# Kernel optimization log

Measured on AMD Instinct MI355X. Metric: run time of the kernel, lower is better.

Reference implementation:

```python
import jax, jax.numpy as jnp
import numpy as np

DIMEN = (341, 341, 341, 341, 341, 343)  # sums to 2048
MARGIN = 0.3
EPS = 1e-12
# index map expanding the 6 per-group attention weights to 2048 feature dims
_EXPAND_IDX = np.repeat(np.arange(len(DIMEN)), DIMEN)  # (2048,)


def setup_inputs() -> dict:
    key = jax.random.key(0)
    k1, k2, k3 = jax.random.split(key, 3)
    inputs = jax.random.normal(k1, (64, 2048), dtype=jnp.float32)
    targets = jax.random.randint(k2, (64,), 0, 16, dtype=jnp.int64)
    attention_attribute = jax.random.uniform(k3, (64, 64, 6), dtype=jnp.float32)
    return {"inputs": inputs, "targets": targets, "attention_attribute": attention_attribute}


def reference(inputs, targets, attention_attribute):
    n = inputs.shape[0]  # 64
    # expand (n,n,6) group weights to (n,n,2048) per-feature weights
    w = attention_attribute[:, :, _EXPAND_IDX]
    # weighted pairwise squared distance: sum_k (w_ijk*(f_jk - f_ik))^2
    diff = inputs[None, :, :] - inputs[:, None, :]  # (n,n,2048)
    sq = jnp.sum((w * diff) ** 2, axis=2)  # (n,n)
    dist = jnp.sqrt(jnp.clip(sq, EPS))  # dist_pos == dist_neg in original
    mask = targets[:, None] == targets[None, :]  # (n,n) bool
    dist_ap = jnp.max(jnp.where(mask, dist, -jnp.inf), axis=1)  # hardest positive
    dist_an = jnp.min(jnp.where(mask, jnp.inf, dist), axis=1)   # hardest negative
    # MarginRankingLoss with y=1: mean(relu(-(dist_an - dist_ap) + margin))
    loss = jnp.mean(jax.nn.relu(dist_ap - dist_an + MARGIN))
    return loss
```

## Files before the change

kernel.cpp:

```cpp
#include <hip/hip_runtime.h>
#include <math.h>


__global__ __launch_bounds__(256) void pair_dist_kernel(
    const float* __restrict__ x,
    const float* __restrict__ attr,
    float* __restrict__ dist)
{
    const int wid  = blockIdx.x * 4 + (threadIdx.x >> 6);
    const int lane = threadIdx.x & 63;
    const int i    = wid >> 6;
    const int j    = wid & 63;

    const float4* __restrict__ xi = (const float4*)(x + i * 2048);
    const float4* __restrict__ xj = (const float4*)(x + j * 2048);
    const float*  __restrict__ a  = attr + wid * 6;

    const float a20 = a[0] * a[0];
    const float a21 = a[1] * a[1];
    const float a22 = a[2] * a[2];
    const float a23 = a[3] * a[3];
    const float a24 = a[4] * a[4];
    const float a25 = a[5] * a[5];

    float acc = 0.f;

#define STEP_B(T, WLO, WHI, B)                                               \
    {                                                                        \
        const int c  = (T) * 64 + lane;                                      \
        const int k0 = c * 4;                                                \
        float4 vi = xi[c];                                                   \
        float4 vj = xj[c];                                                   \
        float dx;                                                            \
        dx = vj.x - vi.x; acc = fmaf(dx * dx, (k0 + 0 < (B)) ? (WLO) : (WHI), acc); \
        dx = vj.y - vi.y; acc = fmaf(dx * dx, (k0 + 1 < (B)) ? (WLO) : (WHI), acc); \
        dx = vj.z - vi.z; acc = fmaf(dx * dx, (k0 + 2 < (B)) ? (WLO) : (WHI), acc); \
        dx = vj.w - vi.w; acc = fmaf(dx * dx, (k0 + 3 < (B)) ? (WLO) : (WHI), acc); \
    }
#define STEP_U(T, W)                                                         \
    {                                                                        \
        const int c = (T) * 64 + lane;                                       \
        float4 vi = xi[c];                                                   \
        float4 vj = xj[c];                                                   \
        float dx;                                                            \
        dx = vj.x - vi.x; acc = fmaf(dx * dx, (W), acc);                     \
        dx = vj.y - vi.y; acc = fmaf(dx * dx, (W), acc);                     \
        dx = vj.z - vi.z; acc = fmaf(dx * dx, (W), acc);                     \
        dx = vj.w - vi.w; acc = fmaf(dx * dx, (W), acc);                     \
    }

    STEP_U(0, a20);
    STEP_B(1, a20, a21, 341);
    STEP_B(2, a21, a22, 682);
    STEP_B(3, a22, a23, 1023);
    STEP_U(4, a23);
    STEP_B(5, a23, a24, 1364);
    STEP_B(6, a24, a25, 1705);
    STEP_U(7, a25);
#undef STEP_B
#undef STEP_U

#pragma unroll
    for (int off = 32; off; off >>= 1) acc += __shfl_xor(acc, off);

    if (lane == 0) dist[wid] = sqrtf(fmaxf(acc, 1e-12f));
}

__global__ __launch_bounds__(1024) void loss_kernel(
    const float* __restrict__ dist,
    const int*   __restrict__ tgt,
    float*       __restrict__ out)
{
    __shared__ float terms[64];
    const int lane = threadIdx.x & 63;
    const int wave = threadIdx.x >> 6;
    const int r0   = wave * 4;

    const int tl = tgt[lane];

    float d0 = dist[(r0 + 0) * 64 + lane];
    float d1 = dist[(r0 + 1) * 64 + lane];
    float d2 = dist[(r0 + 2) * 64 + lane];
    float d3 = dist[(r0 + 3) * 64 + lane];

#define ROW_REDUCE(RR, DV)                                                   \
    {                                                                        \
        const int tr = tgt[RR];                                              \
        bool pos = (tr == tl);                                               \
        float ap = pos ? (DV) : -INFINITY;                                   \
        float an = pos ? INFINITY : (DV);                                    \
        _Pragma("unroll")                                                    \
        for (int off = 32; off; off >>= 1) {                                 \
            ap = fmaxf(ap, __shfl_xor(ap, off));                             \
            an = fminf(an, __shfl_xor(an, off));                             \
        }                                                                    \
        if (lane == 0) terms[RR] = fmaxf(ap - an + 0.3f, 0.f);               \
    }
    ROW_REDUCE(r0 + 0, d0);
    ROW_REDUCE(r0 + 1, d1);
    ROW_REDUCE(r0 + 2, d2);
    ROW_REDUCE(r0 + 3, d3);
#undef ROW_REDUCE

    __syncthreads();

    if (threadIdx.x < 64) {
        float v = terms[threadIdx.x];
#pragma unroll
        for (int off = 32; off; off >>= 1) v += __shfl_xor(v, off);
        if (threadIdx.x == 0) out[0] = v * (1.0f / 64.0f);
    }
}

extern "C" void kernel_launch(void* const* d_in, const int* in_sizes, int n_in,
                              void* d_out, int out_size, void* d_ws, size_t ws_size,
                              hipStream_t stream) {
    const float* x    = (const float*)d_in[0];
    const int*   tgt  = (const int*)d_in[1];
    const float* attr = (const float*)d_in[2];
    float* out  = (float*)d_out;
    float* dist = (float*)d_ws;

    pair_dist_kernel<<<1024, 256, 0, stream>>>(x, attr, dist);
    loss_kernel<<<1, 1024, 0, stream>>>(dist, tgt, out);
}
```

Before: 13.54 us.

## Fuse pairwise distance and loss reduction into one kernel using atomics

Merges the distance kernel and the loss kernel into a single launch. Each block of 16 waves handles one row i and 16 columns j, and reduces its hardest positive and negative locally. It then publishes them with atomicMin on order-preserving float bit patterns, and the last block to finish, found with a global counter, computes the mean margin loss. A hipMemsetAsync on the workspace is added to initialise the atomics and counter, so there are still two stream operations, plus extra atomics and fences.

```diff
diff --git a/kernel.cpp b/kernel.cpp
--- a/kernel.cpp
+++ b/kernel.cpp
@@ -2,19 +2,26 @@
 #include <math.h>
 
 
-__global__ __launch_bounds__(256) void pair_dist_kernel(
-    const float* __restrict__ x,
-    const float* __restrict__ attr,
-    float* __restrict__ dist)
+__global__ __launch_bounds__(1024) void triplet_fused(
+    const float*    __restrict__ x,
+    const int*      __restrict__ tgt,
+    const float*    __restrict__ attr,
+    float*          __restrict__ out,
+    unsigned int*   __restrict__ ws)
 {
-    const int wid  = blockIdx.x * 4 + (threadIdx.x >> 6);
+    const int b    = blockIdx.x;
+    const int i    = b >> 2;
+    const int jc   = b & 3;
+    const int wave = threadIdx.x >> 6;
     const int lane = threadIdx.x & 63;
-    const int i    = wid >> 6;
-    const int j    = wid & 63;
+    const int j    = jc * 16 + wave;
+
+    __shared__ float sm[16];
+    __shared__ int   s_last;
 
     const float4* __restrict__ xi = (const float4*)(x + i * 2048);
     const float4* __restrict__ xj = (const float4*)(x + j * 2048);
-    const float*  __restrict__ a  = attr + wid * 6;
+    const float*  __restrict__ a  = attr + (i * 64 + j) * 6;
 
     const float a20 = a[0] * a[0];
     const float a21 = a[1] * a[1];
@@ -63,52 +70,46 @@
 #pragma unroll
     for (int off = 32; off; off >>= 1) acc += __shfl_xor(acc, off);
 
-    if (lane == 0) dist[wid] = sqrtf(fmaxf(acc, 1e-12f));
-}
-
-__global__ __launch_bounds__(1024) void loss_kernel(
-    const float* __restrict__ dist,
-    const int*   __restrict__ tgt,
-    float*       __restrict__ out)
-{
-    __shared__ float terms[64];
-    const int lane = threadIdx.x & 63;
-    const int wave = threadIdx.x >> 6;
-    const int r0   = wave * 4;
-
-    const int tl = tgt[lane];
-
-    float d0 = dist[(r0 + 0) * 64 + lane];
-    float d1 = dist[(r0 + 1) * 64 + lane];
-    float d2 = dist[(r0 + 2) * 64 + lane];
-    float d3 = dist[(r0 + 3) * 64 + lane];
-
-#define ROW_REDUCE(RR, DV)                                                   \
-    {                                                                        \
-        const int tr = tgt[RR];                                              \
-        bool pos = (tr == tl);                                               \
-        float ap = pos ? (DV) : -INFINITY;                                   \
-        float an = pos ? INFINITY : (DV);                                    \
-        _Pragma("unroll")                                                    \
-        for (int off = 32; off; off >>= 1) {                                 \
-            ap = fmaxf(ap, __shfl_xor(ap, off));                             \
-            an = fminf(an, __shfl_xor(an, off));                             \
-        }                                                                    \
-        if (lane == 0) terms[RR] = fmaxf(ap - an + 0.3f, 0.f);               \
-    }
-    ROW_REDUCE(r0 + 0, d0);
-    ROW_REDUCE(r0 + 1, d1);
-    ROW_REDUCE(r0 + 2, d2);
-    ROW_REDUCE(r0 + 3, d3);
-#undef ROW_REDUCE
+    if (lane == 0) sm[wave] = sqrtf(fmaxf(acc, 1e-12f));
 
     __syncthreads();
 
-    if (threadIdx.x < 64) {
-        float v = terms[threadIdx.x];
+    if (threadIdx.x < 16) {
+        const int   jj  = jc * 16 + threadIdx.x;
+        const float d   = sm[threadIdx.x];
+        const bool  pos = (tgt[jj] == tgt[i]);
+        float apv = pos ? d : -INFINITY;
+        float anv = pos ? INFINITY : d;
 #pragma unroll
-        for (int off = 32; off; off >>= 1) v += __shfl_xor(v, off);
-        if (threadIdx.x == 0) out[0] = v * (1.0f / 64.0f);
+        for (int off = 8; off; off >>= 1) {
+            apv = fmaxf(apv, __shfl_xor(apv, off));
+            anv = fminf(anv, __shfl_xor(anv, off));
+        }
+        if (threadIdx.x == 0) {
+            if (apv >= 0.f) atomicMin(&ws[64 + i], ~__float_as_uint(apv));
+            if (anv < INFINITY) atomicMin(&ws[i], __float_as_uint(anv));
+            __threadfence();
+            const unsigned old = atomicAdd(&ws[128], 1u);
+            s_last = (old == 254u) ? 1 : 0;
+        }
+    }
+    __syncthreads();
+
+    if (s_last) {
+        __threadfence();
+        if (threadIdx.x < 64) {
+            const int r = threadIdx.x;
+            const unsigned anb = __hip_atomic_load(&ws[r], __ATOMIC_RELAXED,
+                                                   __HIP_MEMORY_SCOPE_AGENT);
+            const unsigned apk = __hip_atomic_load(&ws[64 + r], __ATOMIC_RELAXED,
+                                                   __HIP_MEMORY_SCOPE_AGENT);
+            const float ap = __uint_as_float(~apk);
+            const float an = __uint_as_float(anb);
+            float term = fmaxf(ap - an + 0.3f, 0.f);
+#pragma unroll
+            for (int off = 32; off; off >>= 1) term += __shfl_xor(term, off);
+            if (r == 0) out[0] = term * (1.0f / 64.0f);
+        }
     }
 }
 
@@ -118,9 +119,9 @@
     const float* x    = (const float*)d_in[0];
     const int*   tgt  = (const int*)d_in[1];
     const float* attr = (const float*)d_in[2];
-    float* out  = (float*)d_out;
-    float* dist = (float*)d_ws;
+    float* out = (float*)d_out;
+    unsigned int* ws = (unsigned int*)d_ws;
 
-    pair_dist_kernel<<<1024, 256, 0, stream>>>(x, attr, dist);
-    loss_kernel<<<1, 1024, 0, stream>>>(dist, tgt, out);
+    hipMemsetAsync(d_ws, 0xFF, 516, stream);
+    triplet_fused<<<256, 1024, 0, stream>>>(x, tgt, attr, out, ws);
 }
```

Measured after the change: 23.74 us. 1.75x slower.
